# Kernel tuning notes

Measured on AMD Instinct MI355X. Metric: run time of the kernel, lower is better.

## Reference

```python
import jax, jax.numpy as jnp
import numpy as np


def setup_inputs() -> dict:
    key = jax.random.key(0)
    kx, kk, kq, kv = jax.random.split(key, 4)
    B, T, C = 4, 2048, 1024
    scale = 1.0 / np.sqrt(C)
    x = jax.random.normal(kx, (B, T, C), dtype=jnp.float32)
    # nn.Linear(C, C, bias=False): y = x @ W.T, W is [C, C]
    Wk = jax.random.normal(kk, (C, C), dtype=jnp.float32) * scale
    Wq = jax.random.normal(kq, (C, C), dtype=jnp.float32) * scale
    Wv = jax.random.normal(kv, (C, C), dtype=jnp.float32) * scale
    return {"x": x, "Wk": Wk, "Wq": Wq, "Wv": Wv}


def reference(x, Wk, Wq, Wv):
    B, T, C = x.shape
    k = jnp.einsum('btc,dc->btd', x, Wk)  # [B,T,C]
    q = jnp.einsum('btc,dc->btd', x, Wq)
    v = jnp.einsum('btc,dc->btd', x, Wv)
    # full T x T score matrix, scaled by C**-0.5 (note: C, not head_dim split)
    wei = jnp.einsum('btd,bsd->bts', q, k) * (C ** -0.5)  # [B,T,T]
    causal = jnp.tril(jnp.ones((T, T), dtype=bool))
    wei = jnp.where(causal, wei, -jnp.inf)
    wei = jax.nn.softmax(wei, axis=-1)
    # dropout(p=0.1) omitted: reference is eval-mode (identity)
    out = jnp.einsum('bts,bsd->btd', wei, v)  # [B,T,C]
    return out
```

## Files before the change

kernel.cpp:

```cpp
#include <hip/hip_runtime.h>
#include <cstdio>
#include <cmath>

#define TSEQ 2048
#define CDIM 1024
#define NBATCH 4

typedef float f32x4 __attribute__((ext_vector_type(4)));
typedef __bf16 bf16x8 __attribute__((ext_vector_type(8)));
typedef unsigned short u16;
typedef u16 u16x8 __attribute__((ext_vector_type(8)));

__device__ __forceinline__ u16 f2bf(float f) {
  unsigned u = __builtin_bit_cast(unsigned, f);
  unsigned r = (u + 0x7FFFu + ((u >> 16) & 1u)) >> 16;
  return (u16)r;
}

__device__ __forceinline__ void gload_lds16(const void* g, void* l) {
  __builtin_amdgcn_global_load_lds(
      (__attribute__((address_space(1))) void*)g,
      (__attribute__((address_space(3))) void*)l, 16, 0, 0);
}

#define SWZ2(b_) ((b_) ^ ((((b_) >> 7) & 7) << 4))

__device__ __forceinline__ void gemm128(
    const u16* __restrict__ A, const u16* __restrict__ B,
    int lda, int ldb, int m0, int n0, int nT,
    char* smem, f32x4 acc[4][4])
{
  u16* Ab = (u16*)smem;
  u16* Bb = (u16*)(smem + 32768);
  const int tid = threadIdx.x, w = tid >> 6, l = tid & 63;
  const int wr = w >> 1, wc = w & 1;
  const int frow = l & 15, fko = l >> 4;
  const int srow = l >> 3;
  const int scol = ((l & 7) * 8) ^ (((l >> 3) & 7) << 3);

  const u16* gA = A + (size_t)(m0 + w * 32 + srow) * lda + scol;
  const u16* gB = B + (size_t)(n0 + w * 32 + srow) * ldb + scol;

  auto stageA = [&](int t) {
    if (t >= nT) return;
    const u16* s = gA + t * 64;
    u16* d = Ab + (t & 1) * 8192 + w * 2048;
    gload_lds16(s, d);
    gload_lds16(s + (size_t)8 * lda, d + 512);
    gload_lds16(s + (size_t)16 * lda, d + 1024);
    gload_lds16(s + (size_t)24 * lda, d + 1536);
  };
  auto stageB = [&](int t) {
    if (t >= nT) return;
    const u16* s = gB + t * 64;
    u16* d = Bb + (t & 1) * 8192 + w * 2048;
    gload_lds16(s, d);
    gload_lds16(s + (size_t)8 * ldb, d + 512);
    gload_lds16(s + (size_t)16 * ldb, d + 1024);
    gload_lds16(s + (size_t)24 * ldb, d + 1536);
  };

#define AOFF(mf, ks) SWZ2(((wr * 64 + (mf) * 16 + frow) * 128 + (ks) * 64 + fko * 16))
#define BOFF(nf, ks) SWZ2(((wc * 64 + (nf) * 16 + frow) * 128 + (ks) * 64 + fko * 16))

  bf16x8 s0A[4][2], s0B[4][2], s1A[4][2], s1B[4][2];

#define RD(S, T) do {                                                         \
    const char* Ab_ = (const char*)Ab + ((T) & 1) * 16384;                    \
    const char* Bb_ = (const char*)Bb + ((T) & 1) * 16384;                    \
    _Pragma("unroll") for (int nf = 0; nf < 4; ++nf)                          \
    _Pragma("unroll") for (int ks = 0; ks < 2; ++ks)                          \
        S##B[nf][ks] = *(const bf16x8*)(Bb_ + BOFF(nf, ks));                  \
    _Pragma("unroll") for (int mf = 0; mf < 4; ++mf)                          \
    _Pragma("unroll") for (int ks = 0; ks < 2; ++ks)                          \
        S##A[mf][ks] = *(const bf16x8*)(Ab_ + AOFF(mf, ks));                  \
  } while (0)

#define MM(S) do {                                                            \
    __builtin_amdgcn_s_setprio(1);                                            \
    _Pragma("unroll") for (int ks = 0; ks < 2; ++ks)                          \
    _Pragma("unroll") for (int mf = 0; mf < 4; ++mf)                          \
    _Pragma("unroll") for (int nf = 0; nf < 4; ++nf)                          \
        acc[mf][nf] = __builtin_amdgcn_mfma_f32_16x16x32_bf16(                \
            S##A[mf][ks], S##B[nf][ks], acc[mf][nf], 0, 0, 0);                \
    __builtin_amdgcn_s_setprio(0);                                            \
  } while (0)

#define WIN(T, CUR, NXT) do {                                                 \
    if ((T) < nT - 2) asm volatile("s_waitcnt vmcnt(8)" ::: "memory");        \
    else              asm volatile("s_waitcnt vmcnt(0)" ::: "memory");        \
    __builtin_amdgcn_s_barrier();                                             \
    __builtin_amdgcn_sched_barrier(0);                                        \
    if ((T) + 1 < nT) RD(NXT, (T) + 1);                                       \
    MM(CUR);                                                                  \
    asm volatile("s_waitcnt lgkmcnt(0)" ::: "memory");                        \
    __builtin_amdgcn_s_barrier();                                             \
    __builtin_amdgcn_sched_barrier(0);                                        \
    stageB((T) + 3);                                                          \
    stageA((T) + 3);                                                          \
  } while (0)

  stageB(0); stageA(0); stageB(1); stageA(1);
  asm volatile("s_waitcnt vmcnt(8)" ::: "memory");
  __builtin_amdgcn_s_barrier();
  RD(s0, 0);
  asm volatile("s_waitcnt lgkmcnt(0)" ::: "memory");
  __builtin_amdgcn_s_barrier();
  __builtin_amdgcn_sched_barrier(0);
  stageB(2); stageA(2);

#pragma unroll 1
  for (int t = 0; t < nT; t += 2) {
    WIN(t, s0, s1);
    WIN(t + 1, s1, s0);
  }
#undef WIN
#undef MM
#undef RD
#undef AOFF
#undef BOFF
}

#define ACC_ZERO4(acc)                                  \
  _Pragma("unroll") for (int m_ = 0; m_ < 4; ++m_)      \
  _Pragma("unroll") for (int n_ = 0; n_ < 4; ++n_)      \
      acc[m_][n_] = (f32x4){0.f, 0.f, 0.f, 0.f};

__global__ void __launch_bounds__(256) k_cvt_all(
    const float* __restrict__ x, const float* __restrict__ Wk,
    const float* __restrict__ Wq, const float* __restrict__ Wv,
    u16* __restrict__ xb, u16* __restrict__ wb)
{
  const int NX8 = (NBATCH * TSEQ * CDIM) / 8;
  const int NW8 = (CDIM * CDIM) / 8;
  int g = blockIdx.x * 256 + threadIdx.x;
  const float* src; u16* dst; int i;
  if (g < NX8) { src = x; dst = xb; i = g; }
  else {
    int g2 = g - NX8;
    int w = g2 / NW8; i = g2 - w * NW8;
    src = (w == 0) ? Wk : (w == 1) ? Wq : Wv;
    dst = wb + (size_t)w * CDIM * CDIM;
  }
  float4 v0 = ((const float4*)src)[2 * i];
  float4 v1 = ((const float4*)src)[2 * i + 1];
  u16x8 o;
  o[0] = f2bf(v0.x); o[1] = f2bf(v0.y); o[2] = f2bf(v0.z); o[3] = f2bf(v0.w);
  o[4] = f2bf(v1.x); o[5] = f2bf(v1.y); o[6] = f2bf(v1.z); o[7] = f2bf(v1.w);
  *(u16x8*)(dst + (size_t)8 * i) = o;
}

__global__ void __launch_bounds__(256, 2) k_gemm_qkv_t(
    const u16* __restrict__ xb, const u16* __restrict__ wb,
    u16* __restrict__ kb, u16* __restrict__ qb, u16* __restrict__ vt)
{
  extern __shared__ char smem[];
  const int id = blockIdx.x;
  const int xcd = id & 7, loc = id >> 3;
  const int mt = xcd * 8 + (loc & 7);
  const int nt = loc >> 3;
  const int m0 = mt * 128, n0g = nt * 128;

  f32x4 acc[4][4];
  ACC_ZERO4(acc);
  gemm128(xb, wb, CDIM, CDIM, m0, n0g, 16, smem, acc);

  const int tid = threadIdx.x, w = tid >> 6, l = tid & 63;
  const int wr = w >> 1, wc = w & 1;
  const int frow = l & 15, fko = l >> 4;
  const int z = n0g >> 10;
  u16* tile = (u16*)smem;
  __syncthreads();
  if (z < 2) {
    u16* outp = (z == 0) ? kb : qb;
    const float scale = (z == 1) ? 0.03125f : 1.0f;
#pragma unroll
    for (int mf = 0; mf < 4; ++mf)
#pragma unroll
      for (int nf = 0; nf < 4; ++nf) {
        const int rl = wr * 64 + mf * 16 + fko * 4;
        const int cl = wc * 64 + nf * 16 + frow;
#pragma unroll
        for (int j = 0; j < 4; ++j)
          tile[(rl + j) * 136 + cl] = f2bf(acc[mf][nf][j] * scale);
      }
    __syncthreads();
    u16* dst = outp + (size_t)m0 * CDIM + (n0g & 1023);
#pragma unroll
    for (int it = 0; it < 8; ++it) {
      const int idx = it * 256 + tid;
      const int r = idx >> 4, ch = idx & 15;
      *(bf16x8*)(dst + (size_t)r * CDIM + ch * 8) =
          *(const bf16x8*)(tile + r * 136 + ch * 8);
    }
  } else {
#pragma unroll
    for (int mf = 0; mf < 4; ++mf)
#pragma unroll
      for (int nf = 0; nf < 4; ++nf) {
        const int cl = wc * 64 + nf * 16 + frow;
        const int rl = wr * 64 + mf * 16 + fko * 4;
#pragma unroll
        for (int j = 0; j < 4; ++j)
          tile[cl * 136 + rl + j] = f2bf(acc[mf][nf][j]);
      }
    __syncthreads();
    const int b = m0 >> 11, t0 = m0 & 2047;
    const int c0g = n0g - 2048;
    u16* dst = vt + ((size_t)b * CDIM + c0g) * TSEQ + t0;
#pragma unroll
    for (int it = 0; it < 8; ++it) {
      const int idx = it * 256 + tid;
      const int c = idx >> 4, ch = idx & 15;
      *(bf16x8*)(dst + (size_t)c * TSEQ + ch * 8) =
          *(const bf16x8*)(tile + c * 136 + ch * 8);
    }
  }
}

__global__ void __launch_bounds__(256, 2) k_gemm_scores_t(
    const u16* __restrict__ qb, const u16* __restrict__ kb,
    u16* __restrict__ pb, float* __restrict__ rs)
{
  extern __shared__ char smem[];
  const int id = blockIdx.x;
  const int sw = (id & 7) * 68 + (id >> 3);
  const int b = sw / 136;
  const int wq = sw - b * 136;
  int y = (int)((sqrtf(8.f * wq + 1.f) - 1.f) * 0.5f);
  while ((y + 1) * (y + 2) / 2 <= wq) ++y;
  while (y * (y + 1) / 2 > wq) --y;
  const int xt = wq - y * (y + 1) / 2;
  const int m0 = y * 128, n0 = xt * 128;

  const u16* A = qb + (size_t)b * TSEQ * CDIM;
  const u16* B = kb + (size_t)b * TSEQ * CDIM;
  u16* P = pb + (size_t)b * TSEQ * TSEQ;

  f32x4 acc[4][4];
  ACC_ZERO4(acc);
  gemm128(A, B, CDIM, CDIM, m0, n0, 16, smem, acc);

  const int tid = threadIdx.x, w = tid >> 6, l = tid & 63;
  const int wr = w >> 1, wc = w & 1;
  const int frow = l & 15, fko = l >> 4;
  u16* tile = (u16*)smem;
  float* rowpart = (float*)(smem + 34816);

  __syncthreads();
#pragma unroll
  for (int mf = 0; mf < 4; ++mf) {
#pragma unroll
    for (int j = 0; j < 4; ++j) {
      const int rloc = wr * 64 + mf * 16 + fko * 4 + j;
      const int rglob = m0 + rloc;
      float p4 = 0.f;
#pragma unroll
      for (int nf = 0; nf < 4; ++nf) {
        const int cl = wc * 64 + nf * 16 + frow;
        const int c = n0 + cl;
        float e = (c <= rglob) ? __expf(acc[mf][nf][j]) : 0.f;
        p4 += e;
        tile[rloc * 136 + cl] = f2bf(e);
      }
#pragma unroll
      for (int d = 1; d < 16; d <<= 1) p4 += __shfl_xor(p4, d);
      if (frow == 0) rowpart[rloc * 2 + wc] = p4;
    }
  }
  __syncthreads();
  u16* dst = P + (size_t)m0 * TSEQ + n0;
#pragma unroll
  for (int it = 0; it < 8; ++it) {
    const int idx = it * 256 + tid;
    const int r = idx >> 4, ch = idx & 15;
    *(bf16x8*)(dst + (size_t)r * TSEQ + ch * 8) =
        *(const bf16x8*)(tile + r * 136 + ch * 8);
  }
  if (tid < 128)
    rs[((size_t)b * 16 + xt) * TSEQ + m0 + tid] =
        rowpart[tid * 2] + rowpart[tid * 2 + 1];
}

__global__ void __launch_bounds__(256, 2) k_gemm_pv_t(
    const u16* __restrict__ pb, const u16* __restrict__ vt,
    const float* __restrict__ rs, float* __restrict__ out)
{
  extern __shared__ char smem[];
  const int id = blockIdx.x;
  const int n = id & 7, loc = id >> 3;
  int b, mt;
  if (loc < 32) { mt = 15 - (loc & 15); b = loc >> 4; }
  else          { mt = loc & 15;        b = 2 + ((loc - 32) >> 4); }
  const int m0 = mt * 128, n0 = n * 128;
  const int nT = 2 * (mt + 1);

  const u16* A = pb + (size_t)b * TSEQ * TSEQ;
  const u16* B = vt + (size_t)b * CDIM * TSEQ;
  float* O = out + (size_t)b * TSEQ * CDIM;

  f32x4 acc[4][4];
  ACC_ZERO4(acc);
  gemm128(A, B, TSEQ, TSEQ, m0, n0, nT, smem, acc);

  const int tid = threadIdx.x, w = tid >> 6, l = tid & 63;
  const int wr = w >> 1, wc = w & 1;
  const int frow = l & 15, fko = l >> 4;

  __syncthreads();
  float* sinv = (float*)smem;
  if (tid < 128) {
    float s = 0.f;
    const float* p = rs + (size_t)b * 16 * TSEQ + m0 + tid;
    for (int x = 0; x <= mt; ++x) s += p[(size_t)x * TSEQ];
    sinv[tid] = 1.f / s;
  }
  __syncthreads();

#pragma unroll
  for (int mf = 0; mf < 4; ++mf) {
    const int rloc = wr * 64 + mf * 16 + fko * 4;
    const int r = m0 + rloc;
    const float4 iv = *(const float4*)&sinv[rloc];
    const float ivj[4] = {iv.x, iv.y, iv.z, iv.w};
#pragma unroll
    for (int nf = 0; nf < 4; ++nf) {
      const int c = n0 + wc * 64 + nf * 16 + frow;
#pragma unroll
      for (int j = 0; j < 4; ++j)
        O[(size_t)(r + j) * CDIM + c] = acc[mf][nf][j] * ivj[j];
    }
  }
}

extern "C" void kernel_launch(void* const* d_in, const int* in_sizes, int n_in,
                              void* d_out, int out_size, void* d_ws, size_t ws_size,
                              hipStream_t stream) {
  const float* x  = (const float*)d_in[0];
  const float* Wk = (const float*)d_in[1];
  const float* Wq = (const float*)d_in[2];
  const float* Wv = (const float*)d_in[3];
  float* out = (float*)d_out;

  const size_t M = (size_t)NBATCH * TSEQ;

  size_t off = 0;
  auto alloc = [&](size_t bytes) {
    void* p = (char*)d_ws + off;
    off += (bytes + 255) & ~(size_t)255;
    return p;
  };
  u16* xb = (u16*)alloc(M * CDIM * 2);
  u16* wb = (u16*)alloc(3ull * CDIM * CDIM * 2);
  u16* qb = (u16*)alloc(M * CDIM * 2);
  u16* kb = (u16*)alloc(M * CDIM * 2);
  u16* vt = (u16*)alloc(M * CDIM * 2);
  u16* pbuf = (u16*)alloc((size_t)NBATCH * TSEQ * TSEQ * 2);
  float* rs = (float*)alloc((size_t)NBATCH * 16 * TSEQ * 4);
  if (off > ws_size) {
    fprintf(stderr, "kernel_launch: ws too small: need %zu, have %zu\n", off, ws_size);
    return;
  }

  const int NX8 = (NBATCH * TSEQ * CDIM) / 8;
  const int NW8 = (CDIM * CDIM) / 8;
  const int cvtBlocks = (NX8 + 3 * NW8) / 256;

  static_cast<void>(hipFuncSetAttribute(
      reinterpret_cast<const void*>(k_gemm_qkv_t),
      hipFuncAttributeMaxDynamicSharedMemorySize, 65536));
  static_cast<void>(hipFuncSetAttribute(
      reinterpret_cast<const void*>(k_gemm_scores_t),
      hipFuncAttributeMaxDynamicSharedMemorySize, 65536));
  static_cast<void>(hipFuncSetAttribute(
      reinterpret_cast<const void*>(k_gemm_pv_t),
      hipFuncAttributeMaxDynamicSharedMemorySize, 65536));

  k_cvt_all<<<cvtBlocks, 256, 0, stream>>>(x, Wk, Wq, Wv, xb, wb);
  k_gemm_qkv_t<<<1536, 256, 65536, stream>>>(xb, wb, kb, qb, vt);
  k_gemm_scores_t<<<544, 256, 65536, stream>>>(qb, kb, pbuf, rs);
  k_gemm_pv_t<<<512, 256, 65536, stream>>>(pbuf, vt, rs, out);
}
```

Measured before the change: 128.5 us.

## Rewrite QKV projection as 256x256-tile 8-wave GEMM with interleaved staging

New measurement: 141.8 us. 10.3% more time.

```diff
diff --git a/kernel.cpp b/kernel.cpp
--- a/kernel.cpp
+++ b/kernel.cpp
@@ -10,6 +10,7 @@
 typedef __bf16 bf16x8 __attribute__((ext_vector_type(8)));
 typedef unsigned short u16;
 typedef u16 u16x8 __attribute__((ext_vector_type(8)));
+typedef u16 u16x4 __attribute__((ext_vector_type(4)));
 
 __device__ __forceinline__ u16 f2bf(float f) {
   unsigned u = __builtin_bit_cast(unsigned, f);
@@ -150,71 +151,138 @@
   *(u16x8*)(dst + (size_t)8 * i) = o;
 }
 
-__global__ void __launch_bounds__(256, 2) k_gemm_qkv_t(
+__global__ void __launch_bounds__(512) k_gemm_qkv8(
     const u16* __restrict__ xb, const u16* __restrict__ wb,
     u16* __restrict__ kb, u16* __restrict__ qb, u16* __restrict__ vt)
 {
   extern __shared__ char smem[];
+  u16* Ab = (u16*)smem;
+  u16* Bb = (u16*)(smem + 65536);
+
   const int id = blockIdx.x;
   const int xcd = id & 7, loc = id >> 3;
-  const int mt = xcd * 8 + (loc & 7);
-  const int nt = loc >> 3;
-  const int m0 = mt * 128, n0g = nt * 128;
-
-  f32x4 acc[4][4];
-  ACC_ZERO4(acc);
-  gemm128(xb, wb, CDIM, CDIM, m0, n0g, 16, smem, acc);
-
-  const int tid = threadIdx.x, w = tid >> 6, l = tid & 63;
-  const int wr = w >> 1, wc = w & 1;
+  const int mt = xcd * 4 + (loc & 3);
+  const int nt = loc >> 2;
+  const int m0 = mt * 256;
+  const int n0g = nt * 256;
+
+  const int tid = threadIdx.x;
+  const int w = tid >> 6, l = tid & 63;
+  const int wr = w >> 2, wc = w & 3;
   const int frow = l & 15, fko = l >> 4;
+  const int bh = wc >> 1;
+  const int srow = l >> 3;
+  const int scol = ((l & 7) * 8) ^ (((l >> 3) & 7) * 8);
+
+  f32x4 acc[8][4];
+#pragma unroll
+  for (int m_ = 0; m_ < 8; ++m_)
+#pragma unroll
+    for (int n_ = 0; n_ < 4; ++n_) acc[m_][n_] = (f32x4){0.f, 0.f, 0.f, 0.f};
+
+  auto stageA = [&](int t, int half) {
+    const u16* g = xb + (size_t)(m0 + half * 128 + w * 16 + srow) * CDIM + t * 64 + scol;
+    u16* lb = Ab + ((t & 1) * 2 + half) * 8192 + w * 1024;
+    gload_lds16(g, lb);
+    gload_lds16(g + (size_t)8 * CDIM, lb + 512);
+  };
+  auto stageB = [&](int t, int half) {
+    const u16* g = wb + (size_t)(n0g + half * 128 + w * 16 + srow) * CDIM + t * 64 + scol;
+    u16* lb = Bb + ((t & 1) * 2 + half) * 8192 + w * 1024;
+    gload_lds16(g, lb);
+    gload_lds16(g + (size_t)8 * CDIM, lb + 512);
+  };
+  auto stageH = [&](int j) {
+    if (j >= 64) return;
+    const int t = j >> 2, kind = j & 3;
+    if (kind == 0) stageB(t, 0);
+    else if (kind == 1) stageB(t, 1);
+    else if (kind == 2) stageA(t, 0);
+    else stageA(t, 1);
+  };
+
+#define AOFF8(mf, ks) SWZ2((((mf) * 16 + frow) * 128 + (ks) * 64 + fko * 16))
+#define BOFF8(nf, ks) SWZ2((((wc & 1) * 64 + (nf) * 16 + frow) * 128 + (ks) * 64 + fko * 16))
+
+#define PHASE(Q, JS, VM) do {                                                 \
+    bf16x8 afr[2][2];                                                         \
+    _Pragma("unroll") for (int mm = 0; mm < 2; ++mm)                          \
+    _Pragma("unroll") for (int ks = 0; ks < 2; ++ks)                          \
+        afr[mm][ks] = *(const bf16x8*)(Abase + AOFF8(2 * (Q) + mm, ks));      \
+    __builtin_amdgcn_sched_barrier(0);                                        \
+    stageH(JS);                                                               \
+    __builtin_amdgcn_s_barrier();                                             \
+    asm volatile("s_waitcnt lgkmcnt(0)" ::: "memory");                        \
+    __builtin_amdgcn_sched_barrier(0);                                        \
+    __builtin_amdgcn_s_setprio(1);                                            \
+    _Pragma("unroll") for (int ks = 0; ks < 2; ++ks)                          \
+    _Pragma("unroll") for (int mm = 0; mm < 2; ++mm)                          \
+    _Pragma("unroll") for (int nf = 0; nf < 4; ++nf)                          \
+        acc[2 * (Q) + mm][nf] = __builtin_amdgcn_mfma_f32_16x16x32_bf16(      \
+            afr[mm][ks], bfr[nf][ks], acc[2 * (Q) + mm][nf], 0, 0, 0);        \
+    __builtin_amdgcn_s_setprio(0);                                            \
+    if ((VM) == 6) asm volatile("s_waitcnt vmcnt(6)" ::: "memory");           \
+    else if ((VM) == 0) asm volatile("s_waitcnt vmcnt(0)" ::: "memory");      \
+    __builtin_amdgcn_s_barrier();                                             \
+  } while (0)
+
+#define KTILE(T, VM) do {                                                     \
+    const char* Abase = (const char*)Ab + (((T) & 1) * 2 + wr) * 16384;       \
+    const char* Bbase = (const char*)Bb + (((T) & 1) * 2 + bh) * 16384;       \
+    bf16x8 bfr[4][2];                                                         \
+    _Pragma("unroll") for (int nf = 0; nf < 4; ++nf)                          \
+    _Pragma("unroll") for (int ks = 0; ks < 2; ++ks)                          \
+        bfr[nf][ks] = *(const bf16x8*)(Bbase + BOFF8(nf, ks));                \
+    PHASE(0, 4 * (T) + 7, -1);                                                \
+    PHASE(1, 4 * (T) + 8, -1);                                                \
+    PHASE(2, 4 * (T) + 9, -1);                                                \
+    PHASE(3, 4 * (T) + 10, VM);                                               \
+  } while (0)
+
+#pragma unroll
+  for (int j = 0; j < 7; ++j) stageH(j);
+  asm volatile("s_waitcnt vmcnt(6)" ::: "memory");
+  __builtin_amdgcn_s_barrier();
+
+#pragma unroll 1
+  for (int i = 0; i < 7; ++i) { KTILE(2 * i, 6); KTILE(2 * i + 1, 6); }
+  KTILE(14, 0);
+  KTILE(15, -1);
+
+#undef PHASE
+#undef KTILE
+#undef AOFF8
+#undef BOFF8
+
   const int z = n0g >> 10;
-  u16* tile = (u16*)smem;
-  __syncthreads();
   if (z < 2) {
     u16* outp = (z == 0) ? kb : qb;
     const float scale = (z == 1) ? 0.03125f : 1.0f;
-#pragma unroll
-    for (int mf = 0; mf < 4; ++mf)
+    const int nc0 = (n0g & 1023) + wc * 64 + frow;
+    const int r0 = m0 + wr * 128 + fko * 4;
+#pragma unroll
+    for (int mf = 0; mf < 8; ++mf)
 #pragma unroll
       for (int nf = 0; nf < 4; ++nf) {
-        const int rl = wr * 64 + mf * 16 + fko * 4;
-        const int cl = wc * 64 + nf * 16 + frow;
-#pragma unroll
-        for (int j = 0; j < 4; ++j)
-          tile[(rl + j) * 136 + cl] = f2bf(acc[mf][nf][j] * scale);
+        const int r = r0 + mf * 16;
+        const int c = nc0 + nf * 16;
+#pragma unroll
+        for (int j2 = 0; j2 < 4; ++j2)
+          outp[(size_t)(r + j2) * CDIM + c] = f2bf(acc[mf][nf][j2] * scale);
       }
-    __syncthreads();
-    u16* dst = outp + (size_t)m0 * CDIM + (n0g & 1023);
-#pragma unroll
-    for (int it = 0; it < 8; ++it) {
-      const int idx = it * 256 + tid;
-      const int r = idx >> 4, ch = idx & 15;
-      *(bf16x8*)(dst + (size_t)r * CDIM + ch * 8) =
-          *(const bf16x8*)(tile + r * 136 + ch * 8);
-    }
   } else {
-#pragma unroll
-    for (int mf = 0; mf < 4; ++mf)
+    const int b = m0 >> 11;
+    const int tloc0 = (m0 & 2047) + wr * 128 + fko * 4;
+    const int c0 = (n0g - 2048) + wc * 64 + frow;
+#pragma unroll
+    for (int mf = 0; mf < 8; ++mf)
 #pragma unroll
       for (int nf = 0; nf < 4; ++nf) {
-        const int cl = wc * 64 + nf * 16 + frow;
-        const int rl = wr * 64 + mf * 16 + fko * 4;
-#pragma unroll
-        for (int j = 0; j < 4; ++j)
-          tile[cl * 136 + rl + j] = f2bf(acc[mf][nf][j]);
+        u16x4 o;
+        o[0] = f2bf(acc[mf][nf][0]); o[1] = f2bf(acc[mf][nf][1]);
+        o[2] = f2bf(acc[mf][nf][2]); o[3] = f2bf(acc[mf][nf][3]);
+        *(u16x4*)(vt + ((size_t)b * CDIM + c0 + nf * 16) * TSEQ + tloc0 + mf * 16) = o;
       }
-    __syncthreads();
-    const int b = m0 >> 11, t0 = m0 & 2047;
-    const int c0g = n0g - 2048;
-    u16* dst = vt + ((size_t)b * CDIM + c0g) * TSEQ + t0;
-#pragma unroll
-    for (int it = 0; it < 8; ++it) {
-      const int idx = it * 256 + tid;
-      const int c = idx >> 4, ch = idx & 15;
-      *(bf16x8*)(dst + (size_t)c * TSEQ + ch * 8) =
-          *(const bf16x8*)(tile + c * 136 + ch * 8);
-    }
   }
 }
 
@@ -367,8 +435,8 @@
   const int cvtBlocks = (NX8 + 3 * NW8) / 256;
 
   static_cast<void>(hipFuncSetAttribute(
-      reinterpret_cast<const void*>(k_gemm_qkv_t),
-      hipFuncAttributeMaxDynamicSharedMemorySize, 65536));
+      reinterpret_cast<const void*>(k_gemm_qkv8),
+      hipFuncAttributeMaxDynamicSharedMemorySize, 131072));
   static_cast<void>(hipFuncSetAttribute(
       reinterpret_cast<const void*>(k_gemm_scores_t),
       hipFuncAttributeMaxDynamicSharedMemorySize, 65536));
@@ -377,7 +445,7 @@
       hipFuncAttributeMaxDynamicSharedMemorySize, 65536));
 
   k_cvt_all<<<cvtBlocks, 256, 0, stream>>>(x, Wk, Wq, Wv, xb, wb);
-  k_gemm_qkv_t<<<1536, 256, 65536, stream>>>(xb, wb, kb, qb, vt);
+  k_gemm_qkv8<<<384, 512, 131072, stream>>>(xb, wb, kb, qb, vt);
   k_gemm_scores_t<<<544, 256, 65536, stream>>>(qb, kb, pbuf, rs);
   k_gemm_pv_t<<<512, 256, 65536, stream>>>(pbuf, vt, rs, out);
 }
```
